# Optimization experiments

Measured on AMD Instinct MI355X. Metric: run time of the kernel, lower is better.

## Reference

```python
import jax, jax.numpy as jnp
import numpy as np

VOCAB = 50000
D = 256          # vector_dim == hidden size
SEQ = 128
BATCH = 4096
NUM_CLASSES = 5


def setup_inputs() -> dict:
    key = jax.random.key(0)
    ks = jax.random.split(key, 8)
    x = jax.random.randint(ks[0], (BATCH, SEQ), 0, VOCAB, dtype=jnp.int64)
    scale = 1.0 / np.sqrt(D)
    emb = jax.random.normal(ks[1], (VOCAB, D), dtype=jnp.float32)
    emb = emb.at[0].set(0.0)  # padding_idx=0 row is zero
    W_ih = jax.random.uniform(ks[2], (D, D), jnp.float32, -scale, scale)
    W_hh = jax.random.uniform(ks[3], (D, D), jnp.float32, -scale, scale)
    b_ih = jax.random.uniform(ks[4], (D,), jnp.float32, -scale, scale)
    b_hh = jax.random.uniform(ks[5], (D,), jnp.float32, -scale, scale)
    W_cls = jax.random.uniform(ks[6], (NUM_CLASSES, D), jnp.float32, -scale, scale)
    b_cls = jax.random.uniform(ks[7], (NUM_CLASSES,), jnp.float32, -scale, scale)
    return {"x": x, "emb": emb, "W_ih": W_ih, "W_hh": W_hh,
            "b_ih": b_ih, "b_hh": b_hh, "W_cls": W_cls, "b_cls": b_cls}


def reference(x, emb, W_ih, W_hh, b_ih, b_hh, W_cls, b_cls):
    # Embedding lookup: [B, S, D]
    xe = emb[x]
    # Precompute input projections for all timesteps in one GEMM.
    x_proj = jnp.einsum("bsd,hd->bsh", xe, W_ih) + b_ih + b_hh  # [B, S, D]

    def step(h, xp_t):
        h = jnp.tanh(xp_t + h @ W_hh.T)
        return h, None

    h0 = jnp.zeros((x.shape[0], W_hh.shape[0]), dtype=xe.dtype)
    # scan over time axis: [S, B, D]
    h_last, _ = jax.lax.scan(step, h0, jnp.swapaxes(x_proj, 0, 1))
    # classifier on last step
    return h_last @ W_cls.T + b_cls  # [B, 5]
```

## Files before the change

kernel.cpp:

```cpp
#include <hip/hip_runtime.h>


typedef __attribute__((ext_vector_type(8))) short bf16x8;
typedef __attribute__((ext_vector_type(4))) float f32x4;

#define VOCAB 50000
#define NBLK_EMB 512

__device__ __align__(256) unsigned short g_P[VOCAB * 256];

static __device__ __forceinline__ float bf2f(unsigned short u) {
    union { unsigned int i; float f; } v; v.i = ((unsigned int)u) << 16; return v.f;
}
static __device__ __forceinline__ float bfbits2f(unsigned int zext_u16) {
    union { unsigned int i; float f; } v; v.i = zext_u16 << 16; return v.f;
}
static __device__ __forceinline__ unsigned short f2bf_rne(float f) {
    union { float f; unsigned int i; } v; v.f = f;
    unsigned int r = v.i + 0x7FFFu + ((v.i >> 16) & 1u);
    return (unsigned short)(r >> 16);
}
static __device__ __forceinline__ unsigned short f2bf_fast(float f) {
    union { float f; unsigned int i; } v; v.f = f;
    return (unsigned short)((v.i + 0x8000u) >> 16);
}
static __device__ __forceinline__ bf16x8 cvt8(float4 a, float4 b) {
    bf16x8 r;
    r[0] = (short)f2bf_rne(a.x); r[1] = (short)f2bf_rne(a.y);
    r[2] = (short)f2bf_rne(a.z); r[3] = (short)f2bf_rne(a.w);
    r[4] = (short)f2bf_rne(b.x); r[5] = (short)f2bf_rne(b.y);
    r[6] = (short)f2bf_rne(b.z); r[7] = (short)f2bf_rne(b.w);
    return r;
}
static __device__ __forceinline__ bf16x8 load8_bf(const float* __restrict__ p) {
    return cvt8(((const float4*)p)[0], ((const float4*)p)[1]);
}
static __device__ __forceinline__ float fast_tanh(float x) {
    x = __builtin_amdgcn_fmed3f(x, -8.f, 8.f);
    float e = __expf(2.f * x);
    return __builtin_fmaf(-2.f, __builtin_amdgcn_rcpf(e + 1.f), 1.f);
}
static __device__ __forceinline__ void barrier_lds_only() {
    asm volatile("s_waitcnt lgkmcnt(0)\n\ts_barrier" ::: "memory");
}

__global__ __launch_bounds__(256, 2)
void emb_proj_kernel(const float* __restrict__ emb,
                     const float* __restrict__ W_ih,
                     const float* __restrict__ b_ih,
                     const float* __restrict__ b_hh)
{
    const int tid  = threadIdx.x;
    const int lane = tid & 63;
    const int wid  = tid >> 6;
    const int n0   = wid * 64;
    const int l15  = lane & 15;
    const int quad = lane >> 4;

    bf16x8 wf[4][8];
    float  bias[4];
    #pragma unroll
    for (int nt = 0; nt < 4; ++nt) {
        int n = n0 + nt * 16 + l15;
        bias[nt] = b_ih[n] + b_hh[n];
        #pragma unroll
        for (int kt = 0; kt < 8; ++kt)
            wf[nt][kt] = load8_bf(W_ih + n * 256 + quad * 8 + kt * 32);
    }

    for (int tile = blockIdx.x; tile < 3125; tile += NBLK_EMB) {
        const float* arow = emb + ((size_t)tile * 16 + l15) * 256 + quad * 8;
        bf16x8 a[8];
        #pragma unroll
        for (int kt = 0; kt < 8; ++kt)
            a[kt] = load8_bf(arow + kt * 32);

        f32x4 acc[4];
        #pragma unroll
        for (int nt = 0; nt < 4; ++nt) acc[nt] = (f32x4){0.f, 0.f, 0.f, 0.f};
        #pragma unroll
        for (int kt = 0; kt < 8; ++kt) {
            #pragma unroll
            for (int nt = 0; nt < 4; ++nt)
                acc[nt] = __builtin_amdgcn_mfma_f32_16x16x32_bf16(a[kt], wf[nt][kt], acc[nt], 0, 0, 0);
        }

        unsigned short* prow = g_P + ((size_t)tile * 16 + quad * 4) * 256 + n0;
        #pragma unroll
        for (int nt = 0; nt < 4; ++nt) {
            #pragma unroll
            for (int r = 0; r < 4; ++r)
                prow[r * 256 + nt * 16 + l15] = f2bf_rne(acc[nt][r] + bias[nt]);
        }
    }
}

__global__ __launch_bounds__(512, 2)
void rnn_kernel(const int* __restrict__ x,
                const float* __restrict__ W_hh,
                const float* __restrict__ W_cls,
                const float* __restrict__ b_cls,
                float* __restrict__ out)
{
    __shared__ __align__(16) unsigned short h_lds[2][16 * 256];
    __shared__ __align__(16) int tok_t[128 * 16];
    __shared__ __align__(16) float wcls_lds[5 * 256];
    __shared__ float bcls_lds[5];

    const int tid  = threadIdx.x;
    const int lane = tid & 63;
    const int wid  = tid >> 6;
    const int b0   = blockIdx.x * 16;
    const int n0   = wid * 32;
    const int l15  = lane & 15;
    const int quad = lane >> 4;

    bf16x8 wf[2][8];
    #pragma unroll
    for (int nt = 0; nt < 2; ++nt) {
        int n = n0 + nt * 16 + l15;
        #pragma unroll
        for (int kt = 0; kt < 8; ++kt)
            wf[nt][kt] = load8_bf(W_hh + n * 256 + quad * 8 + kt * 32);
    }

    {
        int row = tid & 15, tq = tid >> 4;
        int4 v = *(const int4*)(x + (size_t)(b0 + row) * 128 + tq * 4);
        tok_t[(tq * 4 + 0) * 16 + row] = v.x;
        tok_t[(tq * 4 + 1) * 16 + row] = v.y;
        tok_t[(tq * 4 + 2) * 16 + row] = v.z;
        tok_t[(tq * 4 + 3) * 16 + row] = v.w;
    }
    if (tid < 320) ((float4*)wcls_lds)[tid] = ((const float4*)W_cls)[tid];
    if (tid < 5)   bcls_lds[tid] = b_cls[tid];
    #pragma unroll
    for (int i = 0; i < 4; ++i) ((unsigned int*)h_lds[0])[tid + i * 512] = 0;

    int aoff[8];
    #pragma unroll
    for (int kt = 0; kt < 8; ++kt)
        aoff[kt] = l15 * 512 + (((quad + 4 * kt) ^ l15) << 4);
    int woff[8];
    #pragma unroll
    for (int nt = 0; nt < 2; ++nt)
        #pragma unroll
        for (int r = 0; r < 4; ++r) {
            int row = quad * 4 + r;
            int g   = (n0 >> 3) + nt * 2 + (l15 >> 3);
            woff[nt * 4 + r] = row * 512 + ((g ^ row) << 4) + (l15 & 7) * 2;
        }

    const unsigned int colByte = (unsigned int)(n0 + l15) * 2;

    unsigned int gA[8], gB[8];
    #pragma unroll
    for (int r = 0; r < 4; ++r) {
        const int* xr = x + (size_t)(b0 + quad * 4 + r) * 128;
        const unsigned short* p0 = g_P + (size_t)xr[0] * 256 + n0 + l15;
        const unsigned short* p1 = g_P + (size_t)xr[1] * 256 + n0 + l15;
        gA[r] = p0[0]; gA[4 + r] = p0[16];
        gB[r] = p1[0]; gB[4 + r] = p1[16];
    }
    barrier_lds_only();

    char* const h0 = (char*)&h_lds[0][0];

    auto step = [&](const char* hA, char* hW, unsigned int* g, int t) {
        f32x4 acc0 = { bfbits2f(g[0]), bfbits2f(g[1]), bfbits2f(g[2]), bfbits2f(g[3]) };
        f32x4 acc1 = { bfbits2f(g[4]), bfbits2f(g[5]), bfbits2f(g[6]), bfbits2f(g[7]) };
        if (t + 2 < 128) {
            int4 tk = *(const int4*)&tok_t[(t + 2) * 16 + quad * 4];
            const unsigned short* r0 = (const unsigned short*)((const char*)g_P + ((unsigned int)tk.x * 512 + colByte));
            const unsigned short* r1 = (const unsigned short*)((const char*)g_P + ((unsigned int)tk.y * 512 + colByte));
            const unsigned short* r2 = (const unsigned short*)((const char*)g_P + ((unsigned int)tk.z * 512 + colByte));
            const unsigned short* r3 = (const unsigned short*)((const char*)g_P + ((unsigned int)tk.w * 512 + colByte));
            g[0] = r0[0]; g[4] = r0[16];
            g[1] = r1[0]; g[5] = r1[16];
            g[2] = r2[0]; g[6] = r2[16];
            g[3] = r3[0]; g[7] = r3[16];
        }
        #pragma unroll
        for (int kt = 0; kt < 8; ++kt) {
            bf16x8 a = *(const bf16x8*)(hA + aoff[kt]);
            acc0 = __builtin_amdgcn_mfma_f32_16x16x32_bf16(a, wf[0][kt], acc0, 0, 0, 0);
            acc1 = __builtin_amdgcn_mfma_f32_16x16x32_bf16(a, wf[1][kt], acc1, 0, 0, 0);
        }
        #pragma unroll
        for (int r = 0; r < 4; ++r) {
            *(unsigned short*)(hW + woff[r])     = f2bf_fast(fast_tanh(acc0[r]));
            *(unsigned short*)(hW + woff[4 + r]) = f2bf_fast(fast_tanh(acc1[r]));
        }
    };

    #pragma unroll 1
    for (int t2 = 0; t2 < 64; ++t2) {
        step(h0,        h0 + 8192, gA, 2 * t2);
        barrier_lds_only();
        step(h0 + 8192, h0,        gB, 2 * t2 + 1);
        barrier_lds_only();
    }

    if (tid < 320) {
        int q = tid & 3, p = tid >> 2;
        int row = p / 5, c = p - row * 5;
        float acc = 0.f;
        #pragma unroll
        for (int kk = 0; kk < 64; ++kk) {
            int k = q * 64 + kk;
            int off = row * 512 + ((((k >> 3) ^ row)) << 4) + (k & 7) * 2;
            acc += bf2f(*(const unsigned short*)(h0 + off)) * wcls_lds[c * 256 + k];
        }
        acc += __shfl_xor(acc, 1);
        acc += __shfl_xor(acc, 2);
        if (q == 0) out[(size_t)(b0 + row) * 5 + c] = acc + bcls_lds[c];
    }
}

extern "C" void kernel_launch(void* const* d_in, const int* in_sizes, int n_in,
                              void* d_out, int out_size, void* d_ws, size_t ws_size,
                              hipStream_t stream)
{
    const int*   x     = (const int*)d_in[0];
    const float* emb   = (const float*)d_in[1];
    const float* W_ih  = (const float*)d_in[2];
    const float* W_hh  = (const float*)d_in[3];
    const float* b_ih  = (const float*)d_in[4];
    const float* b_hh  = (const float*)d_in[5];
    const float* W_cls = (const float*)d_in[6];
    const float* b_cls = (const float*)d_in[7];
    float*       out   = (float*)d_out;
    (void)d_ws; (void)ws_size;

    emb_proj_kernel<<<NBLK_EMB, 256, 0, stream>>>(emb, W_ih, b_ih, b_hh);
    rnn_kernel<<<256, 512, 0, stream>>>(x, W_hh, W_cls, b_cls, out);
}
```

Baseline: 258.8 us.

## Stage embedding tiles cooperatively through double-buffered LDS with register prefetch

The embedding-projection kernel used to have every wave load and convert the same 16 embedding rows itself. Now the block loads each tile once with coalesced float4 reads, converts it to bf16 into a padded LDS buffer, and prefetches tiles two iterations ahead in registers, using a fully unrolled loop. The aim is to remove the 4x redundant global traffic and hide load latency, at the cost of an LDS round trip and a barrier per tile. The RNN kernel's LDS-only barriers are also replaced with __syncthreads. On AMD that barrier typically also waits on outstanding global loads, which can expose the latency of the gather prefetch at every timestep.

```diff
diff --git a/kernel.cpp b/kernel.cpp
--- a/kernel.cpp
+++ b/kernel.cpp
@@ -6,6 +6,7 @@
 
 #define VOCAB 50000
 #define NBLK_EMB 512
+#define LDS_STRIDE 264
 
 __device__ __align__(256) unsigned short g_P[VOCAB * 256];
 
@@ -44,16 +45,18 @@
     asm volatile("s_waitcnt lgkmcnt(0)\n\ts_barrier" ::: "memory");
 }
 
-__global__ __launch_bounds__(256, 2)
+__global__ __launch_bounds__(256)
 void emb_proj_kernel(const float* __restrict__ emb,
                      const float* __restrict__ W_ih,
                      const float* __restrict__ b_ih,
                      const float* __restrict__ b_hh)
 {
+    __shared__ __align__(16) unsigned short tin[2][16 * LDS_STRIDE];
     const int tid  = threadIdx.x;
     const int lane = tid & 63;
     const int wid  = tid >> 6;
     const int n0   = wid * 64;
+    const int row  = tid >> 4, seg = tid & 15;
     const int l15  = lane & 15;
     const int quad = lane >> 4;
 
@@ -68,29 +71,49 @@
             wf[nt][kt] = load8_bf(W_ih + n * 256 + quad * 8 + kt * 32);
     }
 
-    for (int tile = blockIdx.x; tile < 3125; tile += NBLK_EMB) {
-        const float* arow = emb + ((size_t)tile * 16 + l15) * 256 + quad * 8;
-        bf16x8 a[8];
-        #pragma unroll
-        for (int kt = 0; kt < 8; ++kt)
-            a[kt] = load8_bf(arow + kt * 32);
-
-        f32x4 acc[4];
-        #pragma unroll
-        for (int nt = 0; nt < 4; ++nt) acc[nt] = (f32x4){0.f, 0.f, 0.f, 0.f};
-        #pragma unroll
-        for (int kt = 0; kt < 8; ++kt) {
+    const int b = blockIdx.x;
+    float4 pf[2][4];
+
+    {
+        const float4* s0 = (const float4*)(emb + ((size_t)b * 16 + row) * 256 + seg * 16);
+        pf[0][0] = s0[0]; pf[0][1] = s0[1]; pf[0][2] = s0[2]; pf[0][3] = s0[3];
+        int t1 = b + NBLK_EMB;
+        if (t1 < 3125) {
+            const float4* s1 = (const float4*)(emb + ((size_t)t1 * 16 + row) * 256 + seg * 16);
+            pf[1][0] = s1[0]; pf[1][1] = s1[1]; pf[1][2] = s1[2]; pf[1][3] = s1[3];
+        }
+    }
+
+    #pragma unroll
+    for (int i = 0; i < 7; ++i) {
+        int tile = b + i * NBLK_EMB;
+        if (tile < 3125) {
+            *(bf16x8*)(&tin[i & 1][row * LDS_STRIDE + seg * 16])     = cvt8(pf[i & 1][0], pf[i & 1][1]);
+            *(bf16x8*)(&tin[i & 1][row * LDS_STRIDE + seg * 16 + 8]) = cvt8(pf[i & 1][2], pf[i & 1][3]);
+            int tf = tile + 2 * NBLK_EMB;
+            if (tf < 3125) {
+                const float4* s = (const float4*)(emb + ((size_t)tf * 16 + row) * 256 + seg * 16);
+                pf[i & 1][0] = s[0]; pf[i & 1][1] = s[1]; pf[i & 1][2] = s[2]; pf[i & 1][3] = s[3];
+            }
+            barrier_lds_only();
+
+            f32x4 acc[4];
             #pragma unroll
-            for (int nt = 0; nt < 4; ++nt)
-                acc[nt] = __builtin_amdgcn_mfma_f32_16x16x32_bf16(a[kt], wf[nt][kt], acc[nt], 0, 0, 0);
-        }
-
-        unsigned short* prow = g_P + ((size_t)tile * 16 + quad * 4) * 256 + n0;
-        #pragma unroll
-        for (int nt = 0; nt < 4; ++nt) {
+            for (int nt = 0; nt < 4; ++nt) acc[nt] = (f32x4){0.f, 0.f, 0.f, 0.f};
             #pragma unroll
-            for (int r = 0; r < 4; ++r)
-                prow[r * 256 + nt * 16 + l15] = f2bf_rne(acc[nt][r] + bias[nt]);
+            for (int kt = 0; kt < 8; ++kt) {
+                bf16x8 a = *(bf16x8*)(&tin[i & 1][l15 * LDS_STRIDE + quad * 8 + kt * 32]);
+                #pragma unroll
+                for (int nt = 0; nt < 4; ++nt)
+                    acc[nt] = __builtin_amdgcn_mfma_f32_16x16x32_bf16(a, wf[nt][kt], acc[nt], 0, 0, 0);
+            }
+            unsigned short* prow = g_P + ((size_t)tile * 16 + quad * 4) * 256 + n0;
+            #pragma unroll
+            for (int nt = 0; nt < 4; ++nt) {
+                #pragma unroll
+                for (int r = 0; r < 4; ++r)
+                    prow[r * 256 + nt * 16 + l15] = f2bf_rne(acc[nt][r] + bias[nt]);
+            }
         }
     }
 }
@@ -162,7 +185,7 @@
         gA[r] = p0[0]; gA[4 + r] = p0[16];
         gB[r] = p1[0]; gB[4 + r] = p1[16];
     }
-    barrier_lds_only();
+    __syncthreads();
 
     char* const h0 = (char*)&h_lds[0][0];
 
@@ -196,9 +219,9 @@
     #pragma unroll 1
     for (int t2 = 0; t2 < 64; ++t2) {
         step(h0,        h0 + 8192, gA, 2 * t2);
-        barrier_lds_only();
+        __syncthreads();
         step(h0 + 8192, h0,        gB, 2 * t2 + 1);
-        barrier_lds_only();
+        __syncthreads();
     }
 
     if (tid < 320) {
```

New measurement: 232.9 us. 10.0% less time.

## Fuse input projection into RNN loop, replace vocab GEMM with bf16 conversion

Applied to the files above, without the earlier changes.

The precomputed 50000-row projection table (emb @ W_ih^T + bias) is dropped. The first kernel now only converts the embedding table to bf16. The RNN kernel gathers each token's full bf16 embedding row one step ahead and computes that step's input projection with extra MFMAs, scheduled after the recurrent MFMAs so they can overlap the tanh and barrier. This removes the vocab-wide GEMM and its bf16 rounding of the projection. The cost is twice the MFMA work per step inside the serial recurrence, full 512-byte row gathers per token instead of two shorts per lane, and more weight registers per thread.

```diff
diff --git a/kernel.cpp b/kernel.cpp
--- a/kernel.cpp
+++ b/kernel.cpp
@@ -5,15 +5,11 @@
 typedef __attribute__((ext_vector_type(4))) float f32x4;
 
 #define VOCAB 50000
-#define NBLK_EMB 512
-
-__device__ __align__(256) unsigned short g_P[VOCAB * 256];
+
+__device__ __align__(256) unsigned short g_E[VOCAB * 256];
 
 static __device__ __forceinline__ float bf2f(unsigned short u) {
     union { unsigned int i; float f; } v; v.i = ((unsigned int)u) << 16; return v.f;
-}
-static __device__ __forceinline__ float bfbits2f(unsigned int zext_u16) {
-    union { unsigned int i; float f; } v; v.i = zext_u16 << 16; return v.f;
 }
 static __device__ __forceinline__ unsigned short f2bf_rne(float f) {
     union { float f; unsigned int i; } v; v.f = f;
@@ -44,60 +40,25 @@
     asm volatile("s_waitcnt lgkmcnt(0)\n\ts_barrier" ::: "memory");
 }
 
-__global__ __launch_bounds__(256, 2)
-void emb_proj_kernel(const float* __restrict__ emb,
-                     const float* __restrict__ W_ih,
-                     const float* __restrict__ b_ih,
-                     const float* __restrict__ b_hh)
+__global__ __launch_bounds__(256)
+void emb_cvt_kernel(const float* __restrict__ emb)
 {
-    const int tid  = threadIdx.x;
-    const int lane = tid & 63;
-    const int wid  = tid >> 6;
-    const int n0   = wid * 64;
-    const int l15  = lane & 15;
-    const int quad = lane >> 4;
-
-    bf16x8 wf[4][8];
-    float  bias[4];
-    #pragma unroll
-    for (int nt = 0; nt < 4; ++nt) {
-        int n = n0 + nt * 16 + l15;
-        bias[nt] = b_ih[n] + b_hh[n];
-        #pragma unroll
-        for (int kt = 0; kt < 8; ++kt)
-            wf[nt][kt] = load8_bf(W_ih + n * 256 + quad * 8 + kt * 32);
-    }
-
-    for (int tile = blockIdx.x; tile < 3125; tile += NBLK_EMB) {
-        const float* arow = emb + ((size_t)tile * 16 + l15) * 256 + quad * 8;
-        bf16x8 a[8];
-        #pragma unroll
-        for (int kt = 0; kt < 8; ++kt)
-            a[kt] = load8_bf(arow + kt * 32);
-
-        f32x4 acc[4];
-        #pragma unroll
-        for (int nt = 0; nt < 4; ++nt) acc[nt] = (f32x4){0.f, 0.f, 0.f, 0.f};
-        #pragma unroll
-        for (int kt = 0; kt < 8; ++kt) {
-            #pragma unroll
-            for (int nt = 0; nt < 4; ++nt)
-                acc[nt] = __builtin_amdgcn_mfma_f32_16x16x32_bf16(a[kt], wf[nt][kt], acc[nt], 0, 0, 0);
-        }
-
-        unsigned short* prow = g_P + ((size_t)tile * 16 + quad * 4) * 256 + n0;
-        #pragma unroll
-        for (int nt = 0; nt < 4; ++nt) {
-            #pragma unroll
-            for (int r = 0; r < 4; ++r)
-                prow[r * 256 + nt * 16 + l15] = f2bf_rne(acc[nt][r] + bias[nt]);
-        }
+    const int nunits = VOCAB * 256 / 8;
+    int gid = blockIdx.x * 256 + threadIdx.x;
+    int stride = gridDim.x * 256;
+    for (int u = gid; u < nunits; u += stride) {
+        const float4* s = (const float4*)(emb + (size_t)u * 8);
+        float4 a = s[0], b = s[1];
+        *(bf16x8*)(g_E + (size_t)u * 8) = cvt8(a, b);
     }
 }
 
 __global__ __launch_bounds__(512, 2)
 void rnn_kernel(const int* __restrict__ x,
+                const float* __restrict__ W_ih,
                 const float* __restrict__ W_hh,
+                const float* __restrict__ b_ih,
+                const float* __restrict__ b_hh,
                 const float* __restrict__ W_cls,
                 const float* __restrict__ b_cls,
                 float* __restrict__ out)
@@ -115,13 +76,17 @@
     const int l15  = lane & 15;
     const int quad = lane >> 4;
 
-    bf16x8 wf[2][8];
+    bf16x8 wfh[2][8], wfi[2][8];
+    float  bias[2];
     #pragma unroll
     for (int nt = 0; nt < 2; ++nt) {
         int n = n0 + nt * 16 + l15;
-        #pragma unroll
-        for (int kt = 0; kt < 8; ++kt)
-            wf[nt][kt] = load8_bf(W_hh + n * 256 + quad * 8 + kt * 32);
+        bias[nt] = b_ih[n] + b_hh[n];
+        #pragma unroll
+        for (int kt = 0; kt < 8; ++kt) {
+            wfh[nt][kt] = load8_bf(W_hh + n * 256 + quad * 8 + kt * 32);
+            wfi[nt][kt] = load8_bf(W_ih + n * 256 + quad * 8 + kt * 32);
+        }
     }
 
     {
@@ -151,54 +116,66 @@
             woff[nt * 4 + r] = row * 512 + ((g ^ row) << 4) + (l15 & 7) * 2;
         }
 
-    const unsigned int colByte = (unsigned int)(n0 + l15) * 2;
-
-    unsigned int gA[8], gB[8];
-    #pragma unroll
-    for (int r = 0; r < 4; ++r) {
-        const int* xr = x + (size_t)(b0 + quad * 4 + r) * 128;
-        const unsigned short* p0 = g_P + (size_t)xr[0] * 256 + n0 + l15;
-        const unsigned short* p1 = g_P + (size_t)xr[1] * 256 + n0 + l15;
-        gA[r] = p0[0]; gA[4 + r] = p0[16];
-        gB[r] = p1[0]; gB[4 + r] = p1[16];
-    }
-    barrier_lds_only();
+    const char* const gE = (const char*)g_E;
+
+    f32x4 xe0, xe1, xo0, xo1;
+    {
+        int tk = x[(size_t)(b0 + l15) * 128];
+        unsigned toff = (unsigned)tk * 512 + quad * 16;
+        bf16x8 e0[8];
+        #pragma unroll
+        for (int kt = 0; kt < 8; ++kt)
+            e0[kt] = *(const bf16x8*)(gE + toff + kt * 64);
+        xe0 = (f32x4){bias[0], bias[0], bias[0], bias[0]};
+        xe1 = (f32x4){bias[1], bias[1], bias[1], bias[1]};
+        #pragma unroll
+        for (int kt = 0; kt < 8; ++kt) {
+            xe0 = __builtin_amdgcn_mfma_f32_16x16x32_bf16(e0[kt], wfi[0][kt], xe0, 0, 0, 0);
+            xe1 = __builtin_amdgcn_mfma_f32_16x16x32_bf16(e0[kt], wfi[1][kt], xe1, 0, 0, 0);
+        }
+    }
+    __syncthreads();
 
     char* const h0 = (char*)&h_lds[0][0];
 
-    auto step = [&](const char* hA, char* hW, unsigned int* g, int t) {
-        f32x4 acc0 = { bfbits2f(g[0]), bfbits2f(g[1]), bfbits2f(g[2]), bfbits2f(g[3]) };
-        f32x4 acc1 = { bfbits2f(g[4]), bfbits2f(g[5]), bfbits2f(g[6]), bfbits2f(g[7]) };
-        if (t + 2 < 128) {
-            int4 tk = *(const int4*)&tok_t[(t + 2) * 16 + quad * 4];
-            const unsigned short* r0 = (const unsigned short*)((const char*)g_P + ((unsigned int)tk.x * 512 + colByte));
-            const unsigned short* r1 = (const unsigned short*)((const char*)g_P + ((unsigned int)tk.y * 512 + colByte));
-            const unsigned short* r2 = (const unsigned short*)((const char*)g_P + ((unsigned int)tk.z * 512 + colByte));
-            const unsigned short* r3 = (const unsigned short*)((const char*)g_P + ((unsigned int)tk.w * 512 + colByte));
-            g[0] = r0[0]; g[4] = r0[16];
-            g[1] = r1[0]; g[5] = r1[16];
-            g[2] = r2[0]; g[6] = r2[16];
-            g[3] = r3[0]; g[7] = r3[16];
+    auto step = [&](const char* hA, char* hW, f32x4& c0, f32x4& c1,
+                    f32x4& p0, f32x4& p1, int t) {
+        bf16x8 eF[8];
+        const bool gg = (t + 1 < 128);
+        if (gg) {
+            int tk = tok_t[(t + 1) * 16 + l15];
+            unsigned toff = (unsigned)tk * 512 + quad * 16;
+            #pragma unroll
+            for (int kt = 0; kt < 8; ++kt)
+                eF[kt] = *(const bf16x8*)(gE + toff + kt * 64);
         }
         #pragma unroll
         for (int kt = 0; kt < 8; ++kt) {
             bf16x8 a = *(const bf16x8*)(hA + aoff[kt]);
-            acc0 = __builtin_amdgcn_mfma_f32_16x16x32_bf16(a, wf[0][kt], acc0, 0, 0, 0);
-            acc1 = __builtin_amdgcn_mfma_f32_16x16x32_bf16(a, wf[1][kt], acc1, 0, 0, 0);
+            c0 = __builtin_amdgcn_mfma_f32_16x16x32_bf16(a, wfh[0][kt], c0, 0, 0, 0);
+            c1 = __builtin_amdgcn_mfma_f32_16x16x32_bf16(a, wfh[1][kt], c1, 0, 0, 0);
         }
         #pragma unroll
         for (int r = 0; r < 4; ++r) {
-            *(unsigned short*)(hW + woff[r])     = f2bf_fast(fast_tanh(acc0[r]));
-            *(unsigned short*)(hW + woff[4 + r]) = f2bf_fast(fast_tanh(acc1[r]));
-        }
+            *(unsigned short*)(hW + woff[r])     = f2bf_fast(fast_tanh(c0[r]));
+            *(unsigned short*)(hW + woff[4 + r]) = f2bf_fast(fast_tanh(c1[r]));
+        }
+        if (gg) {
+            p0 = (f32x4){bias[0], bias[0], bias[0], bias[0]};
+            p1 = (f32x4){bias[1], bias[1], bias[1], bias[1]};
+            #pragma unroll
+            for (int kt = 0; kt < 8; ++kt) {
+                p0 = __builtin_amdgcn_mfma_f32_16x16x32_bf16(eF[kt], wfi[0][kt], p0, 0, 0, 0);
+                p1 = __builtin_amdgcn_mfma_f32_16x16x32_bf16(eF[kt], wfi[1][kt], p1, 0, 0, 0);
+            }
+        }
+        barrier_lds_only();
     };
 
     #pragma unroll 1
     for (int t2 = 0; t2 < 64; ++t2) {
-        step(h0,        h0 + 8192, gA, 2 * t2);
-        barrier_lds_only();
-        step(h0 + 8192, h0,        gB, 2 * t2 + 1);
-        barrier_lds_only();
+        step(h0,        h0 + 8192, xe0, xe1, xo0, xo1, 2 * t2);
+        step(h0 + 8192, h0,        xo0, xo1, xe0, xe1, 2 * t2 + 1);
     }
 
     if (tid < 320) {
@@ -232,6 +209,6 @@
     float*       out   = (float*)d_out;
     (void)d_ws; (void)ws_size;
 
-    emb_proj_kernel<<<NBLK_EMB, 256, 0, stream>>>(emb, W_ih, b_ih, b_hh);
-    rnn_kernel<<<256, 512, 0, stream>>>(x, W_hh, W_cls, b_cls, out);
-}
+    emb_cvt_kernel<<<2048, 256, 0, stream>>>(emb);
+    rnn_kernel<<<256, 512, 0, stream>>>(x, W_ih, W_hh, b_ih, b_hh, W_cls, b_cls, out);
+}
```

After: 409.1 us. 58.1% more time.
